# Optimization experiments

Hardware: AMD Instinct MI355X
Metric: run time of the kernel (lower is better)

## Reference

```python
import jax, jax.numpy as jnp
import numpy as np

N_USERS, N_MOVIES, M, K = 100000, 20000, 8, 32
B = 524288

def setup_inputs() -> dict:
    key = jax.random.key(0)
    k1, k2, k3, k4 = jax.random.split(key, 4)
    edge = jax.random.randint(k1, (B, 2), 0, 20000, dtype=jnp.int64) if jax.config.jax_enable_x64 else jax.random.randint(k1, (B, 2), 0, 20000, dtype=jnp.int32)
    std = 1.0 / K
    taste_emb = jax.random.normal(k2, (N_USERS, M * K), dtype=jnp.float32) * std
    attn_emb = jax.random.normal(k3, (N_USERS, M * K), dtype=jnp.float32) * std
    movie_emb = jax.random.normal(k4, (N_MOVIES, K), dtype=jnp.float32) * std
    user_bias = jnp.zeros((N_USERS, 1), dtype=jnp.float32)
    movie_bias = jnp.zeros((N_MOVIES, 1), dtype=jnp.float32)
    return {"edge": edge, "taste_emb": taste_emb, "attn_emb": attn_emb,
            "movie_emb": movie_emb, "user_bias": user_bias, "movie_bias": movie_bias}

def reference(edge, taste_emb, attn_emb, movie_emb, user_bias, movie_bias):
    u = edge[:, 0]
    v = edge[:, 1]
    A = attn_emb[u].reshape(-1, M, K)   # [B, m, k]
    U = taste_emb[u].reshape(-1, M, K)  # [B, m, k]
    e = movie_emb[v]                    # [B, k]
    logits = jnp.einsum('bmk,bk->bm', A, e)          # bmm(A, e) -> [B, m]
    att = jax.nn.softmax(logits, axis=1)             # softmax over m tastes
    scores = jnp.einsum('bmk,bk->bm', U, e)          # bmm(U, e) -> [B, m]
    y_hat = jnp.sum(scores * att, axis=1) + movie_bias[v, 0] + user_bias[u, 0]
    return y_hat  # [B]
```

## Files before the change

kernel.cpp:

```cpp
#include <hip/hip_runtime.h>


#define MOT_CAP     64
#define MOT_OVF_CAP 4096

using half8 = __attribute__((ext_vector_type(8))) _Float16;
using f32x4 = __attribute__((ext_vector_type(4))) float;

__global__ void mot_zero_kernel(int4* __restrict__ p, int n4) {
    const int i = blockIdx.x * 256 + (int)threadIdx.x;
    if (i < n4) p[i] = make_int4(0, 0, 0, 0);
}

__device__ __forceinline__ float mot_score_div(const float* __restrict__ Ar,
                                               const float* __restrict__ Tr,
                                               const float4* __restrict__ Ep) {
    float4 ek[8];
    #pragma unroll
    for (int k4 = 0; k4 < 8; ++k4) ek[k4] = Ep[k4];
    float num = 0.f, den = 0.f;
    #pragma unroll
    for (int m = 0; m < 8; ++m) {
        float l = 0.f, s = 0.f;
        #pragma unroll
        for (int k4 = 0; k4 < 8; ++k4) {
            const float4 a = *(const float4*)(Ar + m * 32 + k4 * 4);
            const float4 t = *(const float4*)(Tr + m * 32 + k4 * 4);
            const float4 e = ek[k4];
            l = fmaf(a.x, e.x, l); l = fmaf(a.y, e.y, l);
            l = fmaf(a.z, e.z, l); l = fmaf(a.w, e.w, l);
            s = fmaf(t.x, e.x, s); s = fmaf(t.y, e.y, s);
            s = fmaf(t.z, e.z, s); s = fmaf(t.w, e.w, s);
        }
        const float ex = __expf(l);
        den += ex;
        num = fmaf(ex, s, num);
    }
    return num / den;
}

__global__ void mot_scatter_kernel(const int4* __restrict__ edge2,
                                   int* __restrict__ cnt,
                                   int* __restrict__ ovfMeta,
                                   int* __restrict__ ovf,
                                   int2* __restrict__ sve,
                                   int nPairs, int nEdges) {
    const int i = blockIdx.x * 256 + (int)threadIdx.x;
    if (i < nPairs) {
        const int4 q = edge2[i];
        int pos = atomicAdd(&cnt[q.x], 1);
        if (pos < MOT_CAP) sve[(size_t)q.x * MOT_CAP + pos] = make_int2(q.y, 2 * i);
        else { int o = atomicAdd(ovfMeta, 1); if (o < MOT_OVF_CAP) ovf[o] = 2 * i; }
        pos = atomicAdd(&cnt[q.z], 1);
        if (pos < MOT_CAP) sve[(size_t)q.z * MOT_CAP + pos] = make_int2(q.w, 2 * i + 1);
        else { int o = atomicAdd(ovfMeta, 1); if (o < MOT_OVF_CAP) ovf[o] = 2 * i + 1; }
    } else if (i == nPairs && (nEdges & 1)) {
        const int2 e = ((const int2*)edge2)[nEdges - 1];
        int pos = atomicAdd(&cnt[e.x], 1);
        if (pos < MOT_CAP) sve[(size_t)e.x * MOT_CAP + pos] = make_int2(e.y, nEdges - 1);
        else { int o = atomicAdd(ovfMeta, 1); if (o < MOT_OVF_CAP) ovf[o] = nEdges - 1; }
    }
}

__global__ __launch_bounds__(256, 4) void mot_mfma_kernel(
    const int2* __restrict__ edge,
    const float* __restrict__ taste_emb,
    const float* __restrict__ attn_emb,
    const float4* __restrict__ movie_emb,
    const float* __restrict__ user_bias,
    const float* __restrict__ movie_bias,
    const int* __restrict__ cnt,
    const int2* __restrict__ sve,
    const int* __restrict__ ovfMeta,
    const int* __restrict__ ovf,
    float* __restrict__ out,
    int nUsers, int mainBlocks)
{
    const int tid  = (int)threadIdx.x;
    const int lane = tid & 63;

    if ((int)blockIdx.x < mainBlocks) {
        const int u = (int)blockIdx.x * 4 + (tid >> 6);
        if (u >= nUsers) return;
        int n = cnt[u];
        n = n > MOT_CAP ? MOT_CAP : n;
        if (n == 0) return;

        const int row = lane & 15;
        const int kq  = lane >> 4;
        const int k0  = kq * 8;

        const float* rowp = (row < 8)
            ? attn_emb  + (size_t)u * 256 + row * 32 + k0
            : taste_emb + (size_t)u * 256 + (row - 8) * 32 + k0;
        const float4 r0 = *(const float4*)rowp;
        const float4 r1 = *(const float4*)(rowp + 4);
        half8 af;
        af[0] = (_Float16)r0.x; af[1] = (_Float16)r0.y;
        af[2] = (_Float16)r0.z; af[3] = (_Float16)r0.w;
        af[4] = (_Float16)r1.x; af[5] = (_Float16)r1.y;
        af[6] = (_Float16)r1.z; af[7] = (_Float16)r1.w;

        const float ub = user_bias[u];
        const int2* __restrict__ bucket = sve + (size_t)u * MOT_CAP;
        const int hi = kq & 1;

        for (int t = 0; t < n; t += 16) {
            const int ei = t + row;
            const bool valid = ei < n;
            const int2 ve = valid ? bucket[ei] : make_int2(0, -1);

            half8 bf = {};
            if (valid) {
                const float4* __restrict__ Ep = movie_emb + (size_t)ve.x * 8;
                const float4 e0 = Ep[kq * 2];
                const float4 e1 = Ep[kq * 2 + 1];
                bf[0] = (_Float16)e0.x; bf[1] = (_Float16)e0.y;
                bf[2] = (_Float16)e0.z; bf[3] = (_Float16)e0.w;
                bf[4] = (_Float16)e1.x; bf[5] = (_Float16)e1.y;
                bf[6] = (_Float16)e1.z; bf[7] = (_Float16)e1.w;
            }

            f32x4 c = {0.f, 0.f, 0.f, 0.f};
            c = __builtin_amdgcn_mfma_f32_16x16x32_f16(af, bf, c, 0, 0, 0);

            const float o0 = __shfl_xor(c[0], 16);
            const float o1 = __shfl_xor(c[1], 16);
            const float o2 = __shfl_xor(c[2], 16);
            const float o3 = __shfl_xor(c[3], 16);
            float v0 = hi ? o0 : c[0], v1 = hi ? o1 : c[1];
            float v2 = hi ? o2 : c[2], v3 = hi ? o3 : c[3];
            float v4 = hi ? c[0] : o0, v5 = hi ? c[1] : o1;
            float v6 = hi ? c[2] : o2, v7 = hi ? c[3] : o3;
            const float w0 = __shfl_xor(v0, 32), w1 = __shfl_xor(v1, 32);
            const float w2 = __shfl_xor(v2, 32), w3 = __shfl_xor(v3, 32);
            const float w4 = __shfl_xor(v4, 32), w5 = __shfl_xor(v5, 32);
            const float w6 = __shfl_xor(v6, 32), w7 = __shfl_xor(v7, 32);

            if (kq == 0 && valid) {
                float den = 0.f, num = 0.f;
                const float e0x = __expf(v0); den += e0x; num = fmaf(e0x, w0, num);
                const float e1x = __expf(v1); den += e1x; num = fmaf(e1x, w1, num);
                const float e2x = __expf(v2); den += e2x; num = fmaf(e2x, w2, num);
                const float e3x = __expf(v3); den += e3x; num = fmaf(e3x, w3, num);
                const float e4x = __expf(v4); den += e4x; num = fmaf(e4x, w4, num);
                const float e5x = __expf(v5); den += e5x; num = fmaf(e5x, w5, num);
                const float e6x = __expf(v6); den += e6x; num = fmaf(e6x, w6, num);
                const float e7x = __expf(v7); den += e7x; num = fmaf(e7x, w7, num);
                out[ve.y] = num * __builtin_amdgcn_rcpf(den) + ub + movie_bias[ve.x];
            }
        }
    } else {
        int oc = ovfMeta[0];
        if (oc > MOT_OVF_CAP) oc = MOT_OVF_CAP;
        const int oi = ((int)blockIdx.x - mainBlocks) * 256 + tid;
        if (oi < oc) {
            const int eid = ovf[oi];
            const int2 ed = edge[eid];
            out[eid] = mot_score_div(attn_emb  + (size_t)ed.x * 256,
                                     taste_emb + (size_t)ed.x * 256,
                                     movie_emb + (size_t)ed.y * 8)
                       + user_bias[ed.x] + movie_bias[ed.y];
        }
    }
}

__global__ __launch_bounds__(256, 4) void mot_flat_kernel(
    const int2* __restrict__ edge,
    const float4* __restrict__ taste_emb,
    const float4* __restrict__ attn_emb,
    const float4* __restrict__ movie_emb,
    const float* __restrict__ user_bias,
    const float* __restrict__ movie_bias,
    float* __restrict__ out,
    int nEdges)
{
    const int tid  = blockIdx.x * 256 + (int)threadIdx.x;
    const int eid  = tid >> 5;
    const int s    = tid & 31;
    if (eid >= nEdges) return;
    const int2 ed = edge[eid];
    const int u = ed.x, v = ed.y;
    const float4* Ap = attn_emb  + (size_t)u * 64;
    const float4* Tp = taste_emb + (size_t)u * 64;
    const float4* Ep = movie_emb + (size_t)v * 8;
    const float4 a0 = Ap[2 * s], a1 = Ap[2 * s + 1];
    const float4 t0 = Tp[2 * s], t1 = Tp[2 * s + 1];
    const int c = s & 3;
    const float4 e0 = Ep[2 * c], e1 = Ep[2 * c + 1];
    float lp = a0.x*e0.x + a0.y*e0.y + a0.z*e0.z + a0.w*e0.w
             + a1.x*e1.x + a1.y*e1.y + a1.z*e1.z + a1.w*e1.w;
    float sp = t0.x*e0.x + t0.y*e0.y + t0.z*e0.z + t0.w*e0.w
             + t1.x*e1.x + t1.y*e1.y + t1.z*e1.z + t1.w*e1.w;
    lp += __shfl_xor(lp, 1); lp += __shfl_xor(lp, 2);
    sp += __shfl_xor(sp, 1); sp += __shfl_xor(sp, 2);
    const float ex = __expf(lp);
    float den = ex, num = ex * sp;
    den += __shfl_xor(den, 4);  num += __shfl_xor(num, 4);
    den += __shfl_xor(den, 8);  num += __shfl_xor(num, 8);
    den += __shfl_xor(den, 16); num += __shfl_xor(num, 16);
    if (s == 0) out[eid] = num / den + user_bias[u] + movie_bias[v];
}

extern "C" void kernel_launch(void* const* d_in, const int* in_sizes, int n_in,
                              void* d_out, int out_size, void* d_ws, size_t ws_size,
                              hipStream_t stream) {
    const int2*   edge       = (const int2*)d_in[0];
    const float*  taste_emb  = (const float*)d_in[1];
    const float*  attn_emb   = (const float*)d_in[2];
    const float*  movie_emb  = (const float*)d_in[3];
    const float*  user_bias  = (const float*)d_in[4];
    const float*  movie_bias = (const float*)d_in[5];
    float*        out        = (float*)d_out;

    const int nEdges = in_sizes[0] / 2;
    const int NB     = in_sizes[3] / 32;

    auto align256 = [](size_t x) { return (x + 255) & ~(size_t)255; };
    char* ws = (char*)d_ws;

    const size_t o_cnt  = 0;
    const size_t o_meta = align256((size_t)NB * 4);
    const size_t o_ovf  = o_meta + 256;
    const size_t o_sve  = align256(o_ovf + (size_t)MOT_OVF_CAP * 4);
    const size_t need   = o_sve + (size_t)NB * MOT_CAP * 8;

    if (ws_size < need) {
        const int blocks = (nEdges * 32 + 255) / 256;
        mot_flat_kernel<<<blocks, 256, 0, stream>>>(
            edge, (const float4*)taste_emb, (const float4*)attn_emb,
            (const float4*)movie_emb, user_bias, movie_bias, out, nEdges);
        return;
    }

    int*  cnt     = (int*)(ws + o_cnt);
    int*  ovfMeta = (int*)(ws + o_meta);
    int*  ovf     = (int*)(ws + o_ovf);
    int2* sve     = (int2*)(ws + o_sve);

    const int n4 = (int)(o_ovf / 16);
    mot_zero_kernel<<<(n4 + 255) / 256, 256, 0, stream>>>((int4*)ws, n4);

    const int nPairs  = nEdges / 2;
    const int sblocks = (nPairs + 1 + 255) / 256;
    mot_scatter_kernel<<<sblocks, 256, 0, stream>>>(
        (const int4*)edge, cnt, ovfMeta, ovf, sve, nPairs, nEdges);

    const int mainBlocks = (NB + 3) / 4;
    const int ovfBlocks  = MOT_OVF_CAP / 256;
    mot_mfma_kernel<<<mainBlocks + ovfBlocks, 256, 0, stream>>>(
        edge, taste_emb, attn_emb, (const float4*)movie_emb,
        user_bias, movie_bias, cnt, sve, ovfMeta, ovf, out, NB, mainBlocks);
}
```

Measured before the change: 65.48 us.

## Process two users per wavefront with interleaved gathers in MFMA kernel

Each wavefront now handles two users instead of one. It loads both A/T fragments and interleaves the movie-embedding gathers and MFMA tiles for both buckets in one loop, to raise memory-level parallelism and halve the wave count. Launch bounds are raised to allow more resident blocks per CU. The cost is more live registers, and the second user's fragment and bias are read even when that user is past nUsers, which reads out of bounds if the user count is odd.

```diff
diff --git a/kernel.cpp b/kernel.cpp
--- a/kernel.cpp
+++ b/kernel.cpp
@@ -62,7 +62,23 @@
     }
 }
 
-__global__ __launch_bounds__(256, 4) void mot_mfma_kernel(
+__device__ __forceinline__ half8 mot_load_afrag(const float* __restrict__ attn_emb,
+                                                const float* __restrict__ taste_emb,
+                                                int u, int row, int k0) {
+    const float* rowp = (row < 8)
+        ? attn_emb  + (size_t)u * 256 + row * 32 + k0
+        : taste_emb + (size_t)u * 256 + (row - 8) * 32 + k0;
+    const float4 r0 = *(const float4*)rowp;
+    const float4 r1 = *(const float4*)(rowp + 4);
+    half8 af;
+    af[0] = (_Float16)r0.x; af[1] = (_Float16)r0.y;
+    af[2] = (_Float16)r0.z; af[3] = (_Float16)r0.w;
+    af[4] = (_Float16)r1.x; af[5] = (_Float16)r1.y;
+    af[6] = (_Float16)r1.z; af[7] = (_Float16)r1.w;
+    return af;
+}
+
+__global__ __launch_bounds__(256, 6) void mot_mfma2_kernel(
     const int2* __restrict__ edge,
     const float* __restrict__ taste_emb,
     const float* __restrict__ attn_emb,
@@ -80,75 +96,98 @@
     const int lane = tid & 63;
 
     if ((int)blockIdx.x < mainBlocks) {
-        const int u = (int)blockIdx.x * 4 + (tid >> 6);
-        if (u >= nUsers) return;
-        int n = cnt[u];
-        n = n > MOT_CAP ? MOT_CAP : n;
-        if (n == 0) return;
+        const int u0 = ((int)blockIdx.x * 4 + (tid >> 6)) * 2;
+        const int u1 = u0 + 1;
+        if (u0 >= nUsers) return;
 
         const int row = lane & 15;
         const int kq  = lane >> 4;
         const int k0  = kq * 8;
-
-        const float* rowp = (row < 8)
-            ? attn_emb  + (size_t)u * 256 + row * 32 + k0
-            : taste_emb + (size_t)u * 256 + (row - 8) * 32 + k0;
-        const float4 r0 = *(const float4*)rowp;
-        const float4 r1 = *(const float4*)(rowp + 4);
-        half8 af;
-        af[0] = (_Float16)r0.x; af[1] = (_Float16)r0.y;
-        af[2] = (_Float16)r0.z; af[3] = (_Float16)r0.w;
-        af[4] = (_Float16)r1.x; af[5] = (_Float16)r1.y;
-        af[6] = (_Float16)r1.z; af[7] = (_Float16)r1.w;
-
-        const float ub = user_bias[u];
-        const int2* __restrict__ bucket = sve + (size_t)u * MOT_CAP;
-        const int hi = kq & 1;
-
-        for (int t = 0; t < n; t += 16) {
-            const int ei = t + row;
-            const bool valid = ei < n;
-            const int2 ve = valid ? bucket[ei] : make_int2(0, -1);
-
-            half8 bf = {};
-            if (valid) {
-                const float4* __restrict__ Ep = movie_emb + (size_t)ve.x * 8;
-                const float4 e0 = Ep[kq * 2];
-                const float4 e1 = Ep[kq * 2 + 1];
-                bf[0] = (_Float16)e0.x; bf[1] = (_Float16)e0.y;
-                bf[2] = (_Float16)e0.z; bf[3] = (_Float16)e0.w;
-                bf[4] = (_Float16)e1.x; bf[5] = (_Float16)e1.y;
-                bf[6] = (_Float16)e1.z; bf[7] = (_Float16)e1.w;
+        const int hi  = kq & 1;
+
+        int n0 = cnt[u0]; n0 = n0 > MOT_CAP ? MOT_CAP : n0;
+        int n1 = (u1 < nUsers) ? cnt[u1] : 0; n1 = n1 > MOT_CAP ? MOT_CAP : n1;
+        const half8 af0 = mot_load_afrag(attn_emb, taste_emb, u0, row, k0);
+        const half8 af1 = mot_load_afrag(attn_emb, taste_emb, u1, row, k0);
+        const float ub0 = user_bias[u0];
+        const float ub1 = user_bias[u1];
+        const int2* __restrict__ b0 = sve + (size_t)u0 * MOT_CAP;
+        const int2* __restrict__ b1 = sve + (size_t)u1 * MOT_CAP;
+
+        int t0 = 0, t1 = 0;
+        while (t0 < n0 || t1 < n1) {
+            const bool d0 = t0 < n0, d1 = t1 < n1;
+
+            int2 ve0 = make_int2(0, -1), ve1 = make_int2(0, -1);
+            half8 bf0 = {}, bf1 = {};
+            bool val0 = false, val1 = false;
+            if (d0) {
+                const int ei = t0 + row;
+                val0 = ei < n0;
+                if (val0) {
+                    ve0 = b0[ei];
+                    const float4* __restrict__ Ep = movie_emb + (size_t)ve0.x * 8;
+                    const float4 e0 = Ep[kq * 2], e1 = Ep[kq * 2 + 1];
+                    bf0[0] = (_Float16)e0.x; bf0[1] = (_Float16)e0.y;
+                    bf0[2] = (_Float16)e0.z; bf0[3] = (_Float16)e0.w;
+                    bf0[4] = (_Float16)e1.x; bf0[5] = (_Float16)e1.y;
+                    bf0[6] = (_Float16)e1.z; bf0[7] = (_Float16)e1.w;
+                }
             }
-
-            f32x4 c = {0.f, 0.f, 0.f, 0.f};
-            c = __builtin_amdgcn_mfma_f32_16x16x32_f16(af, bf, c, 0, 0, 0);
-
-            const float o0 = __shfl_xor(c[0], 16);
-            const float o1 = __shfl_xor(c[1], 16);
-            const float o2 = __shfl_xor(c[2], 16);
-            const float o3 = __shfl_xor(c[3], 16);
-            float v0 = hi ? o0 : c[0], v1 = hi ? o1 : c[1];
-            float v2 = hi ? o2 : c[2], v3 = hi ? o3 : c[3];
-            float v4 = hi ? c[0] : o0, v5 = hi ? c[1] : o1;
-            float v6 = hi ? c[2] : o2, v7 = hi ? c[3] : o3;
-            const float w0 = __shfl_xor(v0, 32), w1 = __shfl_xor(v1, 32);
-            const float w2 = __shfl_xor(v2, 32), w3 = __shfl_xor(v3, 32);
-            const float w4 = __shfl_xor(v4, 32), w5 = __shfl_xor(v5, 32);
-            const float w6 = __shfl_xor(v6, 32), w7 = __shfl_xor(v7, 32);
-
-            if (kq == 0 && valid) {
-                float den = 0.f, num = 0.f;
-                const float e0x = __expf(v0); den += e0x; num = fmaf(e0x, w0, num);
-                const float e1x = __expf(v1); den += e1x; num = fmaf(e1x, w1, num);
-                const float e2x = __expf(v2); den += e2x; num = fmaf(e2x, w2, num);
-                const float e3x = __expf(v3); den += e3x; num = fmaf(e3x, w3, num);
-                const float e4x = __expf(v4); den += e4x; num = fmaf(e4x, w4, num);
-                const float e5x = __expf(v5); den += e5x; num = fmaf(e5x, w5, num);
-                const float e6x = __expf(v6); den += e6x; num = fmaf(e6x, w6, num);
-                const float e7x = __expf(v7); den += e7x; num = fmaf(e7x, w7, num);
-                out[ve.y] = num * __builtin_amdgcn_rcpf(den) + ub + movie_bias[ve.x];
+            if (d1) {
+                const int ei = t1 + row;
+                val1 = ei < n1;
+                if (val1) {
+                    ve1 = b1[ei];
+                    const float4* __restrict__ Ep = movie_emb + (size_t)ve1.x * 8;
+                    const float4 e0 = Ep[kq * 2], e1 = Ep[kq * 2 + 1];
+                    bf1[0] = (_Float16)e0.x; bf1[1] = (_Float16)e0.y;
+                    bf1[2] = (_Float16)e0.z; bf1[3] = (_Float16)e0.w;
+                    bf1[4] = (_Float16)e1.x; bf1[5] = (_Float16)e1.y;
+                    bf1[6] = (_Float16)e1.z; bf1[7] = (_Float16)e1.w;
+                }
             }
+
+            #pragma unroll
+            for (int g = 0; g < 2; ++g) {
+                const bool dg = g ? d1 : d0;
+                if (!dg) continue;
+                const half8 af = g ? af1 : af0;
+                const half8 bf = g ? bf1 : bf0;
+                const bool val = g ? val1 : val0;
+                const int2 ve = g ? ve1 : ve0;
+                const float ub = g ? ub1 : ub0;
+
+                f32x4 c = {0.f, 0.f, 0.f, 0.f};
+                c = __builtin_amdgcn_mfma_f32_16x16x32_f16(af, bf, c, 0, 0, 0);
+
+                const float o0 = __shfl_xor(c[0], 16);
+                const float o1 = __shfl_xor(c[1], 16);
+                const float o2 = __shfl_xor(c[2], 16);
+                const float o3 = __shfl_xor(c[3], 16);
+                float v0 = hi ? o0 : c[0], v1 = hi ? o1 : c[1];
+                float v2 = hi ? o2 : c[2], v3 = hi ? o3 : c[3];
+                float v4 = hi ? c[0] : o0, v5 = hi ? c[1] : o1;
+                float v6 = hi ? c[2] : o2, v7 = hi ? c[3] : o3;
+                const float w0 = __shfl_xor(v0, 32), w1 = __shfl_xor(v1, 32);
+                const float w2 = __shfl_xor(v2, 32), w3 = __shfl_xor(v3, 32);
+                const float w4 = __shfl_xor(v4, 32), w5 = __shfl_xor(v5, 32);
+                const float w6 = __shfl_xor(v6, 32), w7 = __shfl_xor(v7, 32);
+
+                if (kq == 0 && val) {
+                    float den = 0.f, num = 0.f;
+                    const float e0x = __expf(v0); den += e0x; num = fmaf(e0x, w0, num);
+                    const float e1x = __expf(v1); den += e1x; num = fmaf(e1x, w1, num);
+                    const float e2x = __expf(v2); den += e2x; num = fmaf(e2x, w2, num);
+                    const float e3x = __expf(v3); den += e3x; num = fmaf(e3x, w3, num);
+                    const float e4x = __expf(v4); den += e4x; num = fmaf(e4x, w4, num);
+                    const float e5x = __expf(v5); den += e5x; num = fmaf(e5x, w5, num);
+                    const float e6x = __expf(v6); den += e6x; num = fmaf(e6x, w6, num);
+                    const float e7x = __expf(v7); den += e7x; num = fmaf(e7x, w7, num);
+                    out[ve.y] = num * __builtin_amdgcn_rcpf(den) + ub + movie_bias[ve.x];
+                }
+            }
+            t0 += 16; t1 += 16;
         }
     } else {
         int oc = ovfMeta[0];
@@ -246,9 +285,9 @@
     mot_scatter_kernel<<<sblocks, 256, 0, stream>>>(
         (const int4*)edge, cnt, ovfMeta, ovf, sve, nPairs, nEdges);
 
-    const int mainBlocks = (NB + 3) / 4;
+    const int mainBlocks = (NB + 7) / 8;
     const int ovfBlocks  = MOT_OVF_CAP / 256;
-    mot_mfma_kernel<<<mainBlocks + ovfBlocks, 256, 0, stream>>>(
+    mot_mfma2_kernel<<<mainBlocks + ovfBlocks, 256, 0, stream>>>(
         edge, taste_emb, attn_emb, (const float4*)movie_emb,
         user_bias, movie_bias, cnt, sve, ovfMeta, ovf, out, NB, mainBlocks);
 }
```

Result: no change. 66.23 us (+1.1%).

## Assign one wavefront per 16-edge tile instead of looping per user

Applied to the files above, without the earlier changes.

Each user's bucket of up to 64 edges is split into four 16-edge tiles, and each tile is handled by its own wavefront, replacing the per-user loop. The grid grows fourfold, occupancy hints rise to 8 blocks per CU, and loads are issued before the early-exit check to overlap latency. The softmax reduction is also restructured to shuffle partial sums instead of gathering all eight logits into one lane. The cost is launching many idle wavefronts for users with few edges, plus reloading the user rows once per tile.

```diff
diff --git a/kernel.cpp b/kernel.cpp
--- a/kernel.cpp
+++ b/kernel.cpp
@@ -62,7 +62,7 @@
     }
 }
 
-__global__ __launch_bounds__(256, 4) void mot_mfma_kernel(
+__global__ __launch_bounds__(256, 8) void mot_tile_kernel(
     const int2* __restrict__ edge,
     const float* __restrict__ taste_emb,
     const float* __restrict__ attn_emb,
@@ -74,81 +74,70 @@
     const int* __restrict__ ovfMeta,
     const int* __restrict__ ovf,
     float* __restrict__ out,
-    int nUsers, int mainBlocks)
+    int nUsers, int nMovies, int mainBlocks)
 {
     const int tid  = (int)threadIdx.x;
     const int lane = tid & 63;
 
     if ((int)blockIdx.x < mainBlocks) {
-        const int u = (int)blockIdx.x * 4 + (tid >> 6);
+        const int w = (int)blockIdx.x * 4 + (tid >> 6);
+        const int u = w >> 2;
+        const int T = w & 3;
         if (u >= nUsers) return;
-        int n = cnt[u];
-        n = n > MOT_CAP ? MOT_CAP : n;
-        if (n == 0) return;
 
         const int row = lane & 15;
         const int kq  = lane >> 4;
         const int k0  = kq * 8;
-
+        const int t   = T * 16;
+
+        const int2 ve = sve[(size_t)u * MOT_CAP + t + row];
+        int n = cnt[u]; n = n > MOT_CAP ? MOT_CAP : n;
         const float* rowp = (row < 8)
             ? attn_emb  + (size_t)u * 256 + row * 32 + k0
             : taste_emb + (size_t)u * 256 + (row - 8) * 32 + k0;
         const float4 r0 = *(const float4*)rowp;
         const float4 r1 = *(const float4*)(rowp + 4);
-        half8 af;
+
+        if (t >= n) return;
+        const float ub = user_bias[u];
+
+        const int vx = ((unsigned)ve.x < (unsigned)nMovies) ? ve.x : 0;
+        const float4* __restrict__ Ep = movie_emb + (size_t)vx * 8;
+        const float4 e0 = Ep[kq * 2], e1 = Ep[kq * 2 + 1];
+
+        half8 af, bf;
         af[0] = (_Float16)r0.x; af[1] = (_Float16)r0.y;
         af[2] = (_Float16)r0.z; af[3] = (_Float16)r0.w;
         af[4] = (_Float16)r1.x; af[5] = (_Float16)r1.y;
         af[6] = (_Float16)r1.z; af[7] = (_Float16)r1.w;
-
-        const float ub = user_bias[u];
-        const int2* __restrict__ bucket = sve + (size_t)u * MOT_CAP;
-        const int hi = kq & 1;
-
-        for (int t = 0; t < n; t += 16) {
+        bf[0] = (_Float16)e0.x; bf[1] = (_Float16)e0.y;
+        bf[2] = (_Float16)e0.z; bf[3] = (_Float16)e0.w;
+        bf[4] = (_Float16)e1.x; bf[5] = (_Float16)e1.y;
+        bf[6] = (_Float16)e1.z; bf[7] = (_Float16)e1.w;
+
+        f32x4 c = {0.f, 0.f, 0.f, 0.f};
+        c = __builtin_amdgcn_mfma_f32_16x16x32_f16(af, bf, c, 0, 0, 0);
+
+        const float s0 = __shfl_xor(c[0], 32);
+        const float s1 = __shfl_xor(c[1], 32);
+        const float s2 = __shfl_xor(c[2], 32);
+        const float s3 = __shfl_xor(c[3], 32);
+        const float e0x = __expf(c[0]);
+        const float e1x = __expf(c[1]);
+        const float e2x = __expf(c[2]);
+        const float e3x = __expf(c[3]);
+        float den = e0x + e1x + e2x + e3x;
+        float num = e0x * s0;
+        num = fmaf(e1x, s1, num);
+        num = fmaf(e2x, s2, num);
+        num = fmaf(e3x, s3, num);
+        den += __shfl_xor(den, 16);
+        num += __shfl_xor(num, 16);
+
+        if (kq == 0) {
             const int ei = t + row;
-            const bool valid = ei < n;
-            const int2 ve = valid ? bucket[ei] : make_int2(0, -1);
-
-            half8 bf = {};
-            if (valid) {
-                const float4* __restrict__ Ep = movie_emb + (size_t)ve.x * 8;
-                const float4 e0 = Ep[kq * 2];
-                const float4 e1 = Ep[kq * 2 + 1];
-                bf[0] = (_Float16)e0.x; bf[1] = (_Float16)e0.y;
-                bf[2] = (_Float16)e0.z; bf[3] = (_Float16)e0.w;
-                bf[4] = (_Float16)e1.x; bf[5] = (_Float16)e1.y;
-                bf[6] = (_Float16)e1.z; bf[7] = (_Float16)e1.w;
-            }
-
-            f32x4 c = {0.f, 0.f, 0.f, 0.f};
-            c = __builtin_amdgcn_mfma_f32_16x16x32_f16(af, bf, c, 0, 0, 0);
-
-            const float o0 = __shfl_xor(c[0], 16);
-            const float o1 = __shfl_xor(c[1], 16);
-            const float o2 = __shfl_xor(c[2], 16);
-            const float o3 = __shfl_xor(c[3], 16);
-            float v0 = hi ? o0 : c[0], v1 = hi ? o1 : c[1];
-            float v2 = hi ? o2 : c[2], v3 = hi ? o3 : c[3];
-            float v4 = hi ? c[0] : o0, v5 = hi ? c[1] : o1;
-            float v6 = hi ? c[2] : o2, v7 = hi ? c[3] : o3;
-            const float w0 = __shfl_xor(v0, 32), w1 = __shfl_xor(v1, 32);
-            const float w2 = __shfl_xor(v2, 32), w3 = __shfl_xor(v3, 32);
-            const float w4 = __shfl_xor(v4, 32), w5 = __shfl_xor(v5, 32);
-            const float w6 = __shfl_xor(v6, 32), w7 = __shfl_xor(v7, 32);
-
-            if (kq == 0 && valid) {
-                float den = 0.f, num = 0.f;
-                const float e0x = __expf(v0); den += e0x; num = fmaf(e0x, w0, num);
-                const float e1x = __expf(v1); den += e1x; num = fmaf(e1x, w1, num);
-                const float e2x = __expf(v2); den += e2x; num = fmaf(e2x, w2, num);
-                const float e3x = __expf(v3); den += e3x; num = fmaf(e3x, w3, num);
-                const float e4x = __expf(v4); den += e4x; num = fmaf(e4x, w4, num);
-                const float e5x = __expf(v5); den += e5x; num = fmaf(e5x, w5, num);
-                const float e6x = __expf(v6); den += e6x; num = fmaf(e6x, w6, num);
-                const float e7x = __expf(v7); den += e7x; num = fmaf(e7x, w7, num);
+            if (ei < n)
                 out[ve.y] = num * __builtin_amdgcn_rcpf(den) + ub + movie_bias[ve.x];
-            }
         }
     } else {
         int oc = ovfMeta[0];
@@ -246,9 +235,9 @@
     mot_scatter_kernel<<<sblocks, 256, 0, stream>>>(
         (const int4*)edge, cnt, ovfMeta, ovf, sve, nPairs, nEdges);
 
-    const int mainBlocks = (NB + 3) / 4;
+    const int mainBlocks = NB;
     const int ovfBlocks  = MOT_OVF_CAP / 256;
-    mot_mfma_kernel<<<mainBlocks + ovfBlocks, 256, 0, stream>>>(
+    mot_tile_kernel<<<mainBlocks + ovfBlocks, 256, 0, stream>>>(
         edge, taste_emb, attn_emb, (const float4*)movie_emb,
-        user_bias, movie_bias, cnt, sve, ovfMeta, ovf, out, NB, mainBlocks);
-}
+        user_bias, movie_bias, cnt, sve, ovfMeta, ovf, out, NB, NB, mainBlocks);
+}
```

Result: no change. 64.83 us (-1.0%).
